# Optimization experiments

Hardware: AMD Instinct MI355X
Metric: run time of the kernel (lower is better)

## Reference

```python
import jax, jax.numpy as jnp
import numpy as np

B, T, I, H, BB, O = 128, 1024, 64, 512, 128, 2  # batch, time, input, hidden, backbone_units, phys outputs

def _lecun_tanh(v):
    return 1.7159 * jnp.tanh(0.666 * v)

def setup_inputs() -> dict:
    key = jax.random.key(0)
    ks = jax.random.split(key, 20)
    s = lambda fan_in: 1.0 / np.sqrt(fan_in)
    def lin(k, out_d, in_d):
        return jax.random.uniform(k, (out_d, in_d), jnp.float32, -s(in_d), s(in_d))
    def bias(k, out_d, in_d):
        return jax.random.uniform(k, (out_d,), jnp.float32, -s(in_d), s(in_d))
    return {
        "x": jax.random.normal(ks[0], (B, T, I), jnp.float32),
        # ncps LSTMCell: input_map Linear(I,4H,bias=True), recurrent_map Linear(H,4H,bias=False)
        "lstm_Wi": lin(ks[1], 4 * H, I),
        "lstm_bi": bias(ks[2], 4 * H, I),
        "lstm_Wh": lin(ks[3], 4 * H, H),
        # CfCCell backbone: Linear(I+H, BB) + lecun_tanh
        "bb_W": lin(ks[4], BB, I + H),
        "bb_b": bias(ks[5], BB, I + H),
        # ff1/ff2/time_a/time_b: Linear(BB, H)
        "ff1_W": lin(ks[6], H, BB), "ff1_b": bias(ks[7], H, BB),
        "ff2_W": lin(ks[8], H, BB), "ff2_b": bias(ks[9], H, BB),
        "ta_W": lin(ks[10], H, BB), "ta_b": bias(ks[11], H, BB),
        "tb_W": lin(ks[12], H, BB), "tb_b": bias(ks[13], H, BB),
        # PhysicsHead: Linear(H, O)
        "head_W": lin(ks[14], O, H), "head_b": bias(ks[15], O, H),
    }

def _cfc_scan(x, lstm_Wi, lstm_bi, lstm_Wh, bb_W, bb_b,
              ff1_W, ff1_b, ff2_W, ff2_b, ta_W, ta_b, tb_W, tb_b):
    Bsz = x.shape[0]
    Hd = ff1_W.shape[0]
    ts = jnp.float32(1.0)  # default elapsed time per step in ncps CfC

    def step(carry, xt):
        h, c = carry
        # mixed-memory LSTM gate (forget-gate bias +1.0, per ncps)
        z = xt @ lstm_Wi.T + lstm_bi + h @ lstm_Wh.T
        i_, ig, fg, og = jnp.split(z, 4, axis=-1)
        c_new = c * jax.nn.sigmoid(fg + 1.0) + jnp.tanh(i_) * jax.nn.sigmoid(ig)
        h_lstm = jnp.tanh(c_new) * jax.nn.sigmoid(og)
        # CfC cell (mode='default') on [input, lstm_hidden]
        f = _lecun_tanh(jnp.concatenate([xt, h_lstm], axis=-1) @ bb_W.T + bb_b)
        ff1 = jnp.tanh(f @ ff1_W.T + ff1_b)
        ff2 = jnp.tanh(f @ ff2_W.T + ff2_b)
        t_interp = jax.nn.sigmoid((f @ ta_W.T + ta_b) * ts + (f @ tb_W.T + tb_b))
        h_new = ff1 * (1.0 - t_interp) + t_interp * ff2
        return (h_new, c_new), h_new

    h0 = jnp.zeros((Bsz, Hd), x.dtype)
    c0 = jnp.zeros((Bsz, Hd), x.dtype)
    (h_last, _), h_seq = jax.lax.scan(step, (h0, c0), jnp.swapaxes(x, 0, 1))
    return jnp.swapaxes(h_seq, 0, 1), h_last  # (B,T,H), (B,H)

def reference(x, lstm_Wi, lstm_bi, lstm_Wh, bb_W, bb_b,
              ff1_W, ff1_b, ff2_W, ff2_b, ta_W, ta_b, tb_W, tb_b,
              head_W, head_b):
    h_seq, last_h = _cfc_scan(x, lstm_Wi, lstm_bi, lstm_Wh, bb_W, bb_b,
                              ff1_W, ff1_b, ff2_W, ff2_b, ta_W, ta_b, tb_W, tb_b)
    phys_pred = h_seq @ head_W.T + head_b  # (B,T,O)
    return phys_pred, last_h
```

## Files before the change

kernel.cpp:

```cpp
#include <hip/hip_runtime.h>

#define NB 128
#define TT 1024
#define DI 64
#define DH 512
#define DB 128
#define GZ 2048
#define KZ 576
#define BST 136

typedef unsigned short u16;
typedef unsigned char u8;
typedef unsigned int u32;
typedef unsigned long long u64;

#if defined(__has_builtin)
#if __has_builtin(__builtin_amdgcn_fdot2)
#define HAS_FDOT2 1
#endif
#if __has_builtin(__builtin_amdgcn_sdot4)
#define HAS_SDOT4 1
#endif
#endif

typedef _Float16 half2v __attribute__((ext_vector_type(2)));

__device__ __forceinline__ float bf2f(u16 u) {
  union { u32 i; float f; } v; v.i = ((u32)u) << 16; return v.f;
}
__device__ __forceinline__ float fsig(float x) {
  return __builtin_amdgcn_rcpf(1.f + __expf(-x));
}
__device__ __forceinline__ float ftanh(float x) {
  return 1.f - 2.f * __builtin_amdgcn_rcpf(__expf(2.f * x) + 1.f);
}
__device__ __forceinline__ float dot2p(u32 w, u32 a, float acc) {
#ifdef HAS_FDOT2
  return __builtin_amdgcn_fdot2(__builtin_bit_cast(half2v, w),
                                __builtin_bit_cast(half2v, a), acc, false);
#else
  half2v hw = __builtin_bit_cast(half2v, w), ha = __builtin_bit_cast(half2v, a);
  acc = fmaf((float)hw.x, (float)ha.x, acc);
  return fmaf((float)hw.y, (float)ha.y, acc);
#endif
}
__device__ __forceinline__ int dot4i(u32 w, u32 a, int acc) {
#ifdef HAS_SDOT4
  return __builtin_amdgcn_sdot4((int)w, (int)a, acc, false);
#else
  acc += (((int)(w << 24)) >> 24) * (((int)(a << 24)) >> 24);
  acc += (((int)(w << 16)) >> 24) * (((int)(a << 16)) >> 24);
  acc += (((int)(w << 8))  >> 24) * (((int)(a << 8))  >> 24);
  acc += (((int)w) >> 24)         * (((int)a) >> 24);
  return acc;
#endif
}
__device__ __forceinline__ u32 packf16(float x, float y) {
  half2v h; h.x = (_Float16)x; h.y = (_Float16)y;
  return __builtin_bit_cast(u32, h);
}
__device__ __forceinline__ u16 f16b(float x) {
  _Float16 h = (_Float16)x;
  return __builtin_bit_cast(u16, h);
}

#define O_WZX  256
#define O_WZ8  (O_WZX + 262144)
#define O_SWZ  (O_WZ8 + 1048576)
#define O_BB8  (O_SWZ + 8192)
#define O_SBB  (O_BB8 + 73728)
#define O_FF8  (O_SBB + 512)
#define O_SFF  (O_FF8 + 262144)
#define O_BIF  (O_SFF + 8192)
#define O_FFB  (O_BIF + 8192)
#define O_BBBF (O_FFB + 8192)
#define O_HWP  (O_BBBF + 512)
#define O_HBF  (O_HWP + 2048)
#define WS_NEED ((u64)(O_HBF + 256))

__global__ void detect_kernel(const u16* x, const u16* wi, const u16* wh, int* flag) {
  const int l = threadIdx.x;
  int cnt = (((x[2 * l] >> 7) & 0xFF) < 134)
          + (((wi[2 * l] >> 7) & 0xFF) < 134)
          + (((wh[2 * l] >> 7) & 0xFF) < 134);
#pragma unroll
  for (int off = 32; off > 0; off >>= 1) cnt += __shfl_down(cnt, off, 64);
  if (l == 0) *flag = (cnt >= 180) ? 1 : 0;
}

__device__ __forceinline__ float ldf(int f, const void* s, u32 i) {
  return f ? bf2f(((const u16*)s)[i]) : ((const float*)s)[i];
}

__global__ void pwzx_kernel(const void* Wi, const int* __restrict__ flag,
                            u32* __restrict__ wzxG) {
  const int o = blockIdx.x * 256 + threadIdx.x;
  const int k2 = blockIdx.y;
  const int f = *flag;
  const u32 i = (u32)o * DI + 2 * k2;
  wzxG[(u32)k2 * GZ + (((u32)(o & 511)) << 2) + (o >> 9)] =
      packf16(ldf(f, Wi, i), ldf(f, Wi, i + 1));
}

__global__ void qwz_kernel(const void* Wh, const int* __restrict__ flag,
                           u32* __restrict__ wzG, float* __restrict__ swzG) {
  const int o = blockIdx.x;
  const int l = threadIdx.x;
  const int f = *flag;
  float w[8]; float mx = 0.f;
#pragma unroll
  for (int qq = 0; qq < 2; ++qq) {
    const int q = l + 64 * qq;
#pragma unroll
    for (int e = 0; e < 4; ++e) {
      const float v = ldf(f, Wh, (u32)o * DH + 4 * q + e);
      w[qq * 4 + e] = v; mx = fmaxf(mx, fabsf(v));
    }
  }
#pragma unroll
  for (int off = 32; off > 0; off >>= 1) mx = fmaxf(mx, __shfl_xor(mx, off, 64));
  mx = fmaxf(mx, 1e-20f);
  const float inv = 127.f / mx;
  if (l == 0) swzG[(((u32)(o & 511)) << 2) + (o >> 9)] = mx / (127.f * 127.f);
#pragma unroll
  for (int qq = 0; qq < 2; ++qq) {
    const int q = l + 64 * qq;
    u32 p = 0;
#pragma unroll
    for (int e = 0; e < 4; ++e) {
      int b = (int)rintf(w[qq * 4 + e] * inv);
      b = b > 127 ? 127 : (b < -127 ? -127 : b);
      p |= ((u32)(b & 0xff)) << (8 * e);
    }
    wzG[(u32)q * GZ + (((u32)(o & 511)) << 2) + (o >> 9)] = p;
  }
}

__global__ void qbb_kernel(const void* bb, const int* __restrict__ flag,
                           u32* __restrict__ bb8, float* __restrict__ sbb) {
  const int m = blockIdx.x;
  const int l = threadIdx.x;
  const int f = *flag;
  float mx = 0.f;
#pragma unroll
  for (int q = 0; q < 9; ++q)
    mx = fmaxf(mx, fabsf(ldf(f, bb, (u32)m * KZ + l + 64 * q)));
#pragma unroll
  for (int off = 32; off > 0; off >>= 1) mx = fmaxf(mx, __shfl_xor(mx, off, 64));
  mx = fmaxf(mx, 1e-20f);
  const float inv = 127.f / mx;
  if (l == 0) sbb[m] = mx / 127.f;
  for (int k4 = l; k4 < 144; k4 += 64) {
    u32 p = 0;
#pragma unroll
    for (int e = 0; e < 4; ++e) {
      int b = (int)rintf(ldf(f, bb, (u32)m * KZ + 4 * k4 + e) * inv);
      b = b > 127 ? 127 : (b < -127 ? -127 : b);
      p |= ((u32)(b & 0xff)) << (8 * e);
    }
    bb8[(u32)k4 * DB + m] = p;
  }
}

__global__ void qff_kernel(const void* f1, const void* f2, const void* ta,
                           const void* tb, const int* __restrict__ flag,
                           u32* __restrict__ ffG, float* __restrict__ sffG) {
  const int o = blockIdx.x;
  const int mat = blockIdx.y;
  const int l = threadIdx.x;
  const void* s = (mat == 0) ? f1 : (mat == 1) ? f2 : (mat == 2) ? ta : tb;
  const int f = *flag;
  float w[4]; float mx = 0.f;
#pragma unroll
  for (int e = 0; e < 4; ++e) {
    w[e] = ldf(f, s, (u32)o * DB + 4 * l + e);
    mx = fmaxf(mx, fabsf(w[e]));
  }
#pragma unroll
  for (int off = 16; off > 0; off >>= 1) mx = fmaxf(mx, __shfl_xor(mx, off, 32));
  mx = fmaxf(mx, 1e-20f);
  const float inv = 127.f / mx;
  if (l == 0) sffG[((u32)o << 2) + mat] = (mx / 127.f) * (1.7159f / 127.f);
  u32 p = 0;
#pragma unroll
  for (int e = 0; e < 4; ++e) {
    int b = (int)rintf(w[e] * inv);
    b = b > 127 ? 127 : (b < -127 ? -127 : b);
    p |= ((u32)(b & 0xff)) << (8 * e);
  }
  ffG[(((u32)l * 512 + o) << 2) + mat] = p;
}

__global__ void psmall_kernel(const void* bi_s, const void* f1b_s, const void* f2b_s,
                              const void* tab_s, const void* tbb_s, const void* bbb_s,
                              const void* hw_s, const void* hb_s,
                              const int* __restrict__ flag,
                              float* __restrict__ bif, float* __restrict__ ffb,
                              float* __restrict__ bbbf, u32* __restrict__ hwp,
                              float* __restrict__ hbf) {
  const int f = *flag;
  for (int i = threadIdx.x; i < 2048; i += 1024) {
    bif[i] = ldf(f, bi_s, i);
    if (i < 512) {
      ffb[i]        = ldf(f, f1b_s, i);
      ffb[512 + i]  = ldf(f, f2b_s, i);
      ffb[1024 + i] = ldf(f, tab_s, i);
      ffb[1536 + i] = ldf(f, tbb_s, i);
      const int w = i >> 8, pr = i & 255;
      hwp[i] = packf16(ldf(f, hw_s, w * DH + 2 * pr), ldf(f, hw_s, w * DH + 2 * pr + 1));
    }
    if (i < 128) bbbf[i] = ldf(f, bbb_s, i);
    if (i < 2)   hbf[i] = ldf(f, hb_s, i);
  }
}

__global__ __launch_bounds__(1024, 1)
void scan18(const void* __restrict__ xraw, const int* __restrict__ flagp,
            const u32* __restrict__ wzxG, const u32* __restrict__ wzG,
            const float* __restrict__ swzG,
            const u32* __restrict__ bb8, const float* __restrict__ sbb,
            const u32* __restrict__ ffG, const float* __restrict__ sffG,
            const float* __restrict__ bif, const float* __restrict__ ffbv,
            const float* __restrict__ bbbf, const u32* __restrict__ hwp,
            const float* __restrict__ hbf, float* __restrict__ out)
{
  __shared__ __align__(16) u32   xf16q[32];
  __shared__ __align__(16) u32   ah8q[128];
  __shared__ __align__(16) u32   hfR[256];
  __shared__ __align__(16) u32   vcat8[144];
  __shared__ __align__(16) float sxq[4];
  __shared__ __align__(16) u32   Fq8[32];
  __shared__ __align__(16) u32   bbL[144 * BST + 1024];

  const int j = threadIdx.x;
  const int b = blockIdx.x;
  const int bf16in = *flagp;
  const int u = j & 511;

  float c0 = 0.f;
  float bgi = 0, bgg = 0, bgf = 0, bgo = 0, cb1 = 0, cb2 = 0, cba = 0, cbb = 0;
  float4 zscl = make_float4(0, 0, 0, 0), sfv = make_float4(0, 0, 0, 0);
  if (j < 512) {
    bgi = bif[0 * DH + u]; bgg = bif[1 * DH + u];
    bgf = bif[2 * DH + u]; bgo = bif[3 * DH + u];
    cb1 = ffbv[0 * DH + u]; cb2 = ffbv[1 * DH + u];
    cba = ffbv[2 * DH + u]; cbb = ffbv[3 * DH + u];
    zscl = *(const float4*)(swzG + 4 * u);
    sfv  = *(const float4*)(sffG + 4 * u);
  }
  float sbbr = 0.f, bbr = 0.f;
  if (j < 512) { sbbr = sbb[j >> 2]; bbr = bbbf[j >> 2]; }
  u32 hwreg[4] = {0, 0, 0, 0}; float hbr = 0.f;
  int hw_ = 0, hl = 0;
  if (j >= 576 && j < 704) {
    const int jj = j - 576;
    hw_ = jj >> 6; hl = jj & 63;
#pragma unroll
    for (int i = 0; i < 4; ++i) hwreg[i] = hwp[hw_ * 256 + hl + 64 * i];
    hbr = hbf[hw_];
  }
  const float C127 = 1.f / 127.f;

  for (int idx = j; idx < 144 * DB; idx += 1024) {
    const int q = idx >> 7, m = idx & 127;
    bbL[q * BST + m] = bb8[idx];
  }

  if (j < 256) { hfR[j] = 0u; if (j < 128) ah8q[j] = 0u; }
  if (j >= 512 && j < 544) {
    const int k2 = j - 512;
    const size_t xi = ((size_t)b * TT + 0) * 32 + k2;
    float a, bb_;
    if (bf16in) {
      const u32 w = ((const u32*)xraw)[xi];
      a = bf2f((u16)(w & 0xffffu)); bb_ = bf2f((u16)(w >> 16));
    } else {
      const float2 v = ((const float2*)xraw)[xi];
      a = v.x; bb_ = v.y;
    }
    xf16q[k2] = packf16(a, bb_);
    float m = fmaxf(fabsf(a), fabsf(bb_));
#pragma unroll
    for (int off = 16; off > 0; off >>= 1) m = fmaxf(m, __shfl_xor(m, off, 32));
    m = fmaxf(m, 1e-20f);
    if (k2 == 0) sxq[0] = m * C127;
    const float inv = 127.f / m;
    const int q0 = (int)rintf(a * inv), q1 = (int)rintf(bb_ * inv);
    ((u16*)vcat8)[k2] = (u16)((q0 & 0xff) | ((q1 & 0xff) << 8));
  }
  __syncthreads();

  for (int t = 0; t < TT; ++t) {
    if (j < 512) {
      float xi0 = 0, xg0 = 0, xf0 = 0, xo0 = 0;
      const u32* wpx = wzxG + 4 * u;
#pragma unroll 8
      for (int k2 = 0; k2 < 32; ++k2) {
        const uint4 w = *(const uint4*)wpx; wpx += GZ;
        const u32 a0 = xf16q[k2];
        xi0 = dot2p(w.x, a0, xi0); xg0 = dot2p(w.y, a0, xg0);
        xf0 = dot2p(w.z, a0, xf0); xo0 = dot2p(w.w, a0, xo0);
      }
      int ii0 = 0, ig0 = 0, if0 = 0, io0 = 0;
      const u32* wph = wzG + 4 * u;
#pragma unroll 8
      for (int q = 0; q < 128; ++q) {
        const uint4 w = *(const uint4*)wph; wph += GZ;
        const u32 a0 = ah8q[q];
        ii0 = dot4i(w.x, a0, ii0); ig0 = dot4i(w.y, a0, ig0);
        if0 = dot4i(w.z, a0, if0); io0 = dot4i(w.w, a0, io0);
      }
      const float zi0 = bgi + xi0 + zscl.x * (float)ii0;
      const float zg0 = bgg + xg0 + zscl.y * (float)ig0;
      const float zf0 = bgf + xf0 + zscl.z * (float)if0;
      const float zo0 = bgo + xo0 + zscl.w * (float)io0;
      c0 = fmaf(c0, fsig(zf0 + 1.f), ftanh(zi0) * fsig(zg0));
      const float hl0 = ftanh(c0) * fsig(zo0);
      const int q0 = (int)rintf(hl0 * 127.f);
      ((u8*)vcat8)[64 + u] = (u8)(q0 & 0xff);
    }
    __syncthreads();

    if (j < 512) {
      const int m = j >> 2, s4 = j & 3;
      const int qb = s4 * 36;
      int ax0 = 0, ah0 = 0;
#pragma unroll 12
      for (int q = 0; q < 36; ++q) {
        const int qq = qb + q;
        const u32 w = bbL[qq * BST + m];
        const int d0 = dot4i(w, vcat8[qq], 0);
        const bool isx = qq < 16;
        ax0 += isx ? d0 : 0; ah0 += isx ? 0 : d0;
      }
      ax0 += __shfl_xor(ax0, 1, 64); ax0 += __shfl_xor(ax0, 2, 64);
      ah0 += __shfl_xor(ah0, 1, 64); ah0 += __shfl_xor(ah0, 2, 64);
      if (s4 == 0) {
        const float r0 = bbr + sbbr * (sxq[0] * (float)ax0 + C127 * (float)ah0);
        const float F0 = 1.7159f * ftanh(0.666f * r0);
        const int q0 = (int)rintf(F0 * (127.f / 1.7159f));
        ((u8*)Fq8)[m] = (u8)(q0 & 0xff);
      }
    }
    __syncthreads();

    if (j < 512) {
      int a10 = 0, a20 = 0, aa0 = 0, ab0 = 0;
      const u32* fw = ffG + 4 * u;
#pragma unroll 8
      for (int l = 0; l < 32; ++l) {
        const uint4 w = *(const uint4*)fw; fw += GZ;
        const u32 F0v = Fq8[l];
        a10 = dot4i(w.x, F0v, a10); a20 = dot4i(w.y, F0v, a20);
        aa0 = dot4i(w.z, F0v, aa0); ab0 = dot4i(w.w, F0v, ab0);
      }
      const float z10 = sfv.x * (float)a10 + cb1, z20 = sfv.y * (float)a20 + cb2;
      const float za0 = sfv.z * (float)aa0 + cba, zb0 = sfv.w * (float)ab0 + cbb;
      const float ti0 = fsig(za0 + zb0);
      const float hn0 = fmaf(ftanh(z10), 1.f - ti0, ti0 * ftanh(z20));
      ((u16*)hfR)[u] = f16b(hn0);
      const int q0 = (int)rintf(hn0 * 127.f);
      ((u8*)ah8q)[u] = (u8)(q0 & 0xff);
      if (t == TT - 1) {
        out[(size_t)NB * TT * 2 + (size_t)b * DH + u] = hn0;
      }
    } else if (j < 544 && t + 1 < TT) {
      const int k2 = j - 512;
      const size_t xi = ((size_t)b * TT + (t + 1)) * 32 + k2;
      float a, bb_;
      if (bf16in) {
        const u32 w = ((const u32*)xraw)[xi];
        a = bf2f((u16)(w & 0xffffu)); bb_ = bf2f((u16)(w >> 16));
      } else {
        const float2 v = ((const float2*)xraw)[xi];
        a = v.x; bb_ = v.y;
      }
      xf16q[k2] = packf16(a, bb_);
      float m = fmaxf(fabsf(a), fabsf(bb_));
#pragma unroll
      for (int off = 16; off > 0; off >>= 1) m = fmaxf(m, __shfl_xor(m, off, 32));
      m = fmaxf(m, 1e-20f);
      if (k2 == 0) sxq[0] = m * C127;
      const float inv = 127.f / m;
      const int q0 = (int)rintf(a * inv), q1 = (int)rintf(bb_ * inv);
      ((u16*)vcat8)[k2] = (u16)((q0 & 0xff) | ((q1 & 0xff) << 8));
    }
    __syncthreads();

    if (j >= 576 && j < 704) {
      float acc = 0.f;
#pragma unroll
      for (int i = 0; i < 4; ++i)
        acc = dot2p(hwreg[i], hfR[hl + 64 * i], acc);
#pragma unroll
      for (int off = 32; off > 0; off >>= 1) acc += __shfl_down(acc, off, 64);
      if (hl == 0) out[((size_t)b * TT + t) * 2 + hw_] = acc + hbr;
    }
  }
}

__device__ __forceinline__ void fma8(float& acc, const uint4 u, const float* v) {
  union { u32 i; float f; } tt;
  tt.i = u.x << 16;          acc = fmaf(tt.f, v[0], acc);
  tt.i = u.x & 0xffff0000u;  acc = fmaf(tt.f, v[1], acc);
  tt.i = u.y << 16;          acc = fmaf(tt.f, v[2], acc);
  tt.i = u.y & 0xffff0000u;  acc = fmaf(tt.f, v[3], acc);
  tt.i = u.z << 16;          acc = fmaf(tt.f, v[4], acc);
  tt.i = u.z & 0xffff0000u;  acc = fmaf(tt.f, v[5], acc);
  tt.i = u.w << 16;          acc = fmaf(tt.f, v[6], acc);
  tt.i = u.w & 0xffff0000u;  acc = fmaf(tt.f, v[7], acc);
}
__global__ __launch_bounds__(256, 1)
void fb_scan(const u16* __restrict__ x,   const u16* __restrict__ Wi,
             const u16* __restrict__ bi,  const u16* __restrict__ Wh,
             const u16* __restrict__ bbW, const u16* __restrict__ bbb,
             const u16* __restrict__ f1W, const u16* __restrict__ f1b,
             const u16* __restrict__ f2W, const u16* __restrict__ f2b,
             const u16* __restrict__ taW, const u16* __restrict__ tab,
             const u16* __restrict__ tbW, const u16* __restrict__ tbb,
             const u16* __restrict__ hW,  const u16* __restrict__ hb,
             float* __restrict__ out)
{
  __shared__ __align__(16) float vcat[DI + DH];
  __shared__ __align__(16) float Fb2[DB];
  __shared__ __align__(16) float fpart[256];
  __shared__ __align__(16) float hprev[DH];
  const int j = threadIdx.x, b = blockIdx.x;
  const int u0 = j, u1 = j + 256;
  float bi_r[8];
#pragma unroll
  for (int k = 0; k < 8; ++k) bi_r[k] = bf2f(bi[j + 256 * k]);
  const float b_f1_0 = bf2f(f1b[u0]), b_f1_1 = bf2f(f1b[u1]);
  const float b_f2_0 = bf2f(f2b[u0]), b_f2_1 = bf2f(f2b[u1]);
  const float b_ta_0 = bf2f(tab[u0]), b_ta_1 = bf2f(tab[u1]);
  const float b_tb_0 = bf2f(tbb[u0]), b_tb_1 = bf2f(tbb[u1]);
  const float b_bb = (j < DB) ? bf2f(bbb[j]) : 0.f;
  float hwr[8]; float hbr = 0.f;
  if (j < 128) {
    const int w = j >> 6, l = j & 63;
#pragma unroll
    for (int q = 0; q < 8; ++q) hwr[q] = bf2f(hW[w * DH + q * 64 + l]);
    hbr = bf2f(hb[w]);
  }
  float c0 = 0.f, c1 = 0.f;
  hprev[u0] = 0.f; hprev[u1] = 0.f;
  const u16* xp = x + (size_t)b * TT * DI;
  __syncthreads();
  for (int t = 0; t < TT; ++t) {
    if (j < DI) vcat[j] = bf2f(xp[t * DI + j]);
    __syncthreads();
    float a[8];
#pragma unroll
    for (int k = 0; k < 8; ++k) a[k] = bi_r[k];
#pragma unroll
    for (int r = 0; r < 8; ++r) {
      const u16* wr = Wi + ((size_t)(j + 256 * r)) * DI;
      float acc = a[r];
#pragma unroll
      for (int kk = 0; kk < DI; kk += 8) fma8(acc, *(const uint4*)(wr + kk), vcat + kk);
      a[r] = acc;
    }
#pragma unroll 1
    for (int kb = 0; kb < DH; kb += 64) {
      float hreg[64];
#pragma unroll
      for (int q = 0; q < 16; ++q)
        *(float4*)(hreg + 4 * q) = *(const float4*)(hprev + kb + 4 * q);
#pragma unroll
      for (int r = 0; r < 8; ++r) {
        const u16* wr = Wh + ((size_t)(j + 256 * r)) * DH + kb;
        float acc = a[r];
#pragma unroll
        for (int cc = 0; cc < 8; ++cc) fma8(acc, *(const uint4*)(wr + 8 * cc), hreg + 8 * cc);
        a[r] = acc;
      }
    }
    {
      const float cn0 = fmaf(c0, fsig(a[4] + 1.f), ftanh(a[0]) * fsig(a[2]));
      const float cn1 = fmaf(c1, fsig(a[5] + 1.f), ftanh(a[1]) * fsig(a[3]));
      c0 = cn0; c1 = cn1;
      vcat[DI + u0] = ftanh(cn0) * fsig(a[6]);
      vcat[DI + u1] = ftanh(cn1) * fsig(a[7]);
    }
    __syncthreads();
    {
      const int mm = j & (DB - 1), pp = j >> 7;
      const u16* br = bbW + (size_t)mm * KZ + pp * 288;
      const float* vs = vcat + pp * 288;
      float s0 = 0.f, s1 = 0.f, s2v = 0.f, s3 = 0.f;
#pragma unroll
      for (int kk = 0; kk < 288; kk += 32) {
        fma8(s0, *(const uint4*)(br + kk), vs + kk);
        fma8(s1, *(const uint4*)(br + kk + 8), vs + kk + 8);
        fma8(s2v, *(const uint4*)(br + kk + 16), vs + kk + 16);
        fma8(s3, *(const uint4*)(br + kk + 24), vs + kk + 24);
      }
      fpart[j] = (s0 + s1) + (s2v + s3);
    }
    __syncthreads();
    if (j < DB) Fb2[j] = 1.7159f * ftanh(0.666f * (b_bb + fpart[j] + fpart[j + DB]));
    __syncthreads();
    {
      float Fr[DB];
#pragma unroll
      for (int q = 0; q < 32; ++q) *(float4*)(Fr + 4 * q) = *(const float4*)(Fb2 + 4 * q);
      const u16* rp[8] = {
        f1W + (size_t)u0 * DB, f1W + (size_t)u1 * DB,
        f2W + (size_t)u0 * DB, f2W + (size_t)u1 * DB,
        taW + (size_t)u0 * DB, taW + (size_t)u1 * DB,
        tbW + (size_t)u0 * DB, tbW + (size_t)u1 * DB };
      float sacc[8] = { b_f1_0, b_f1_1, b_f2_0, b_f2_1, b_ta_0, b_ta_1, b_tb_0, b_tb_1 };
#pragma unroll
      for (int rr = 0; rr < 8; ++rr) {
        float acc = sacc[rr];
        const u16* r = rp[rr];
#pragma unroll
        for (int kk = 0; kk < DB; kk += 8) fma8(acc, *(const uint4*)(r + kk), Fr + kk);
        sacc[rr] = acc;
      }
      const float ti0 = fsig(sacc[4] + sacc[6]);
      const float ti1 = fsig(sacc[5] + sacc[7]);
      hprev[u0] = fmaf(ftanh(sacc[0]), 1.f - ti0, ti0 * ftanh(sacc[2]));
      hprev[u1] = fmaf(ftanh(sacc[1]), 1.f - ti1, ti1 * ftanh(sacc[3]));
    }
    __syncthreads();
    if (j < 128) {
      const int l = j & 63;
      float acc = 0.f;
#pragma unroll
      for (int q = 0; q < 8; ++q) acc = fmaf(hprev[q * 64 + l], hwr[q], acc);
#pragma unroll
      for (int off = 32; off > 0; off >>= 1) acc += __shfl_down(acc, off, 64);
      if (l == 0) out[((size_t)b * TT + t) * 2 + (j >> 6)] = acc + hbr;
    }
  }
  out[(size_t)NB * TT * 2 + (size_t)b * DH + u0] = hprev[u0];
  out[(size_t)NB * TT * 2 + (size_t)b * DH + u1] = hprev[u1];
}

extern "C" void kernel_launch(void* const* d_in, const int* in_sizes, int n_in,
                              void* d_out, int out_size, void* d_ws, size_t ws_size,
                              hipStream_t stream) {
  (void)in_sizes; (void)n_in; (void)out_size;

  if (ws_size >= WS_NEED) {
    char* ws = (char*)d_ws;
    int* flag = (int*)ws;
    detect_kernel<<<dim3(1), dim3(64), 0, stream>>>(
        (const u16*)d_in[0], (const u16*)d_in[1], (const u16*)d_in[3], flag);
    pwzx_kernel<<<dim3(8, 32), dim3(256), 0, stream>>>(d_in[1], flag, (u32*)(ws + O_WZX));
    qwz_kernel<<<dim3(2048), dim3(64), 0, stream>>>(d_in[3], flag,
                                                    (u32*)(ws + O_WZ8), (float*)(ws + O_SWZ));
    qbb_kernel<<<dim3(128), dim3(64), 0, stream>>>(d_in[4], flag,
                                                   (u32*)(ws + O_BB8), (float*)(ws + O_SBB));
    qff_kernel<<<dim3(512, 4), dim3(32), 0, stream>>>(d_in[6], d_in[8], d_in[10],
                                                      d_in[12], flag,
                                                      (u32*)(ws + O_FF8), (float*)(ws + O_SFF));
    psmall_kernel<<<dim3(1), dim3(1024), 0, stream>>>(
        d_in[2], d_in[7], d_in[9], d_in[11], d_in[13], d_in[5], d_in[14], d_in[15],
        flag, (float*)(ws + O_BIF), (float*)(ws + O_FFB), (float*)(ws + O_BBBF),
        (u32*)(ws + O_HWP), (float*)(ws + O_HBF));

    scan18<<<dim3(128), dim3(1024), 0, stream>>>(
        d_in[0], flag,
        (const u32*)(ws + O_WZX), (const u32*)(ws + O_WZ8), (const float*)(ws + O_SWZ),
        (const u32*)(ws + O_BB8), (const float*)(ws + O_SBB),
        (const u32*)(ws + O_FF8), (const float*)(ws + O_SFF),
        (const float*)(ws + O_BIF), (const float*)(ws + O_FFB),
        (const float*)(ws + O_BBBF), (const u32*)(ws + O_HWP),
        (const float*)(ws + O_HBF), (float*)d_out);
  } else {
    fb_scan<<<dim3(NB), dim3(256), 0, stream>>>(
        (const u16*)d_in[0],  (const u16*)d_in[1],  (const u16*)d_in[2],
        (const u16*)d_in[3],  (const u16*)d_in[4],  (const u16*)d_in[5],
        (const u16*)d_in[6],  (const u16*)d_in[7],  (const u16*)d_in[8],
        (const u16*)d_in[9],  (const u16*)d_in[10], (const u16*)d_in[11],
        (const u16*)d_in[12], (const u16*)d_in[13], (const u16*)d_in[14],
        (const u16*)d_in[15], (float*)d_out);
  }
}
```

Measured before the change: 13.20 ms.

## Compute input projection for two timesteps per weight load and separate x/h backbone buffers

The x@Wi projection now runs every other step and computes both the current and next timestep from the same global weight loads, keeping the next step's result in registers. This halves weight streaming for that part of the recurrence. The x prefetch moves two steps ahead into a 4-slot ring buffer so both steps' inputs are ready. The backbone dot product now uses separate x-int8 and h-int8 buffers with split loops, which removes the per-iteration select. The cost is more registers per thread and an uneven amount of work on odd and even steps.

```diff
diff --git a/kernel.cpp b/kernel.cpp
--- a/kernel.cpp
+++ b/kernel.cpp
@@ -215,7 +215,7 @@
 }
 
 __global__ __launch_bounds__(1024, 1)
-void scan18(const void* __restrict__ xraw, const int* __restrict__ flagp,
+void scan19(const void* __restrict__ xraw, const int* __restrict__ flagp,
             const u32* __restrict__ wzxG, const u32* __restrict__ wzG,
             const float* __restrict__ swzG,
             const u32* __restrict__ bb8, const float* __restrict__ sbb,
@@ -224,10 +224,11 @@
             const float* __restrict__ bbbf, const u32* __restrict__ hwp,
             const float* __restrict__ hbf, float* __restrict__ out)
 {
-  __shared__ __align__(16) u32   xf16q[32];
+  __shared__ __align__(16) u32   xf16q[128];
+  __shared__ __align__(16) u32   xi8q[64];
+  __shared__ __align__(16) u32   hl8q[128];
   __shared__ __align__(16) u32   ah8q[128];
   __shared__ __align__(16) u32   hfR[256];
-  __shared__ __align__(16) u32   vcat8[144];
   __shared__ __align__(16) float sxq[4];
   __shared__ __align__(16) u32   Fq8[32];
   __shared__ __align__(16) u32   bbL[144 * BST + 1024];
@@ -238,6 +239,7 @@
   const int u = j & 511;
 
   float c0 = 0.f;
+  float sxi = 0.f, sxg = 0.f, sxf = 0.f, sxo = 0.f;
   float bgi = 0, bgg = 0, bgf = 0, bgo = 0, cb1 = 0, cb2 = 0, cba = 0, cbb = 0;
   float4 zscl = make_float4(0, 0, 0, 0), sfv = make_float4(0, 0, 0, 0);
   if (j < 512) {
@@ -267,9 +269,9 @@
   }
 
   if (j < 256) { hfR[j] = 0u; if (j < 128) ah8q[j] = 0u; }
-  if (j >= 512 && j < 544) {
-    const int k2 = j - 512;
-    const size_t xi = ((size_t)b * TT + 0) * 32 + k2;
+  if (j >= 512 && j < 576) {
+    const int s = (j - 512) >> 5, k2 = (j - 512) & 31;
+    const size_t xi = ((size_t)b * TT + s) * 32 + k2;
     float a, bb_;
     if (bf16in) {
       const u32 w = ((const u32*)xraw)[xi];
@@ -278,29 +280,20 @@
       const float2 v = ((const float2*)xraw)[xi];
       a = v.x; bb_ = v.y;
     }
-    xf16q[k2] = packf16(a, bb_);
+    xf16q[s * 32 + k2] = packf16(a, bb_);
     float m = fmaxf(fabsf(a), fabsf(bb_));
 #pragma unroll
     for (int off = 16; off > 0; off >>= 1) m = fmaxf(m, __shfl_xor(m, off, 32));
     m = fmaxf(m, 1e-20f);
-    if (k2 == 0) sxq[0] = m * C127;
+    if (k2 == 0) sxq[s] = m * C127;
     const float inv = 127.f / m;
     const int q0 = (int)rintf(a * inv), q1 = (int)rintf(bb_ * inv);
-    ((u16*)vcat8)[k2] = (u16)((q0 & 0xff) | ((q1 & 0xff) << 8));
+    ((u16*)xi8q)[s * 32 + k2] = (u16)((q0 & 0xff) | ((q1 & 0xff) << 8));
   }
   __syncthreads();
 
   for (int t = 0; t < TT; ++t) {
     if (j < 512) {
-      float xi0 = 0, xg0 = 0, xf0 = 0, xo0 = 0;
-      const u32* wpx = wzxG + 4 * u;
-#pragma unroll 8
-      for (int k2 = 0; k2 < 32; ++k2) {
-        const uint4 w = *(const uint4*)wpx; wpx += GZ;
-        const u32 a0 = xf16q[k2];
-        xi0 = dot2p(w.x, a0, xi0); xg0 = dot2p(w.y, a0, xg0);
-        xf0 = dot2p(w.z, a0, xf0); xo0 = dot2p(w.w, a0, xo0);
-      }
       int ii0 = 0, ig0 = 0, if0 = 0, io0 = 0;
       const u32* wph = wzG + 4 * u;
 #pragma unroll 8
@@ -310,6 +303,26 @@
         ii0 = dot4i(w.x, a0, ii0); ig0 = dot4i(w.y, a0, ig0);
         if0 = dot4i(w.z, a0, if0); io0 = dot4i(w.w, a0, io0);
       }
+      float xi0, xg0, xf0, xo0;
+      if ((t & 1) == 0) {
+        xi0 = 0; xg0 = 0; xf0 = 0; xo0 = 0;
+        float xiN = 0, xgN = 0, xfN = 0, xoN = 0;
+        const u32* wpx = wzxG + 4 * u;
+        const u32* xc = xf16q + (t & 3) * 32;
+        const u32* xn = xf16q + ((t + 1) & 3) * 32;
+#pragma unroll 8
+        for (int k2 = 0; k2 < 32; ++k2) {
+          const uint4 w = *(const uint4*)wpx; wpx += GZ;
+          const u32 a0 = xc[k2], a1 = xn[k2];
+          xi0 = dot2p(w.x, a0, xi0); xg0 = dot2p(w.y, a0, xg0);
+          xf0 = dot2p(w.z, a0, xf0); xo0 = dot2p(w.w, a0, xo0);
+          xiN = dot2p(w.x, a1, xiN); xgN = dot2p(w.y, a1, xgN);
+          xfN = dot2p(w.z, a1, xfN); xoN = dot2p(w.w, a1, xoN);
+        }
+        sxi = xiN; sxg = xgN; sxf = xfN; sxo = xoN;
+      } else {
+        xi0 = sxi; xg0 = sxg; xf0 = sxf; xo0 = sxo;
+      }
       const float zi0 = bgi + xi0 + zscl.x * (float)ii0;
       const float zg0 = bgg + xg0 + zscl.y * (float)ig0;
       const float zf0 = bgf + xf0 + zscl.z * (float)if0;
@@ -317,26 +330,28 @@
       c0 = fmaf(c0, fsig(zf0 + 1.f), ftanh(zi0) * fsig(zg0));
       const float hl0 = ftanh(c0) * fsig(zo0);
       const int q0 = (int)rintf(hl0 * 127.f);
-      ((u8*)vcat8)[64 + u] = (u8)(q0 & 0xff);
+      ((u8*)hl8q)[u] = (u8)(q0 & 0xff);
     }
     __syncthreads();
 
     if (j < 512) {
       const int m = j >> 2, s4 = j & 3;
-      const int qb = s4 * 36;
       int ax0 = 0, ah0 = 0;
-#pragma unroll 12
-      for (int q = 0; q < 36; ++q) {
-        const int qq = qb + q;
-        const u32 w = bbL[qq * BST + m];
-        const int d0 = dot4i(w, vcat8[qq], 0);
-        const bool isx = qq < 16;
-        ax0 += isx ? d0 : 0; ah0 += isx ? 0 : d0;
+      const u32* xq = xi8q + (t & 3) * 16;
+#pragma unroll
+      for (int q = 0; q < 4; ++q) {
+        const int qq = 4 * q + s4;
+        ax0 = dot4i(bbL[qq * BST + m], xq[qq], ax0);
+      }
+#pragma unroll 8
+      for (int q = 4; q < 36; ++q) {
+        const int qq = 4 * q + s4;
+        ah0 = dot4i(bbL[qq * BST + m], hl8q[qq - 16], ah0);
       }
       ax0 += __shfl_xor(ax0, 1, 64); ax0 += __shfl_xor(ax0, 2, 64);
       ah0 += __shfl_xor(ah0, 1, 64); ah0 += __shfl_xor(ah0, 2, 64);
       if (s4 == 0) {
-        const float r0 = bbr + sbbr * (sxq[0] * (float)ax0 + C127 * (float)ah0);
+        const float r0 = bbr + sbbr * (sxq[t & 3] * (float)ax0 + C127 * (float)ah0);
         const float F0 = 1.7159f * ftanh(0.666f * r0);
         const int q0 = (int)rintf(F0 * (127.f / 1.7159f));
         ((u8*)Fq8)[m] = (u8)(q0 & 0xff);
@@ -364,9 +379,10 @@
       if (t == TT - 1) {
         out[(size_t)NB * TT * 2 + (size_t)b * DH + u] = hn0;
       }
-    } else if (j < 544 && t + 1 < TT) {
+    } else if (j < 544 && t + 2 < TT) {
       const int k2 = j - 512;
-      const size_t xi = ((size_t)b * TT + (t + 1)) * 32 + k2;
+      const int slot = (t + 2) & 3;
+      const size_t xi = ((size_t)b * TT + (t + 2)) * 32 + k2;
       float a, bb_;
       if (bf16in) {
         const u32 w = ((const u32*)xraw)[xi];
@@ -375,15 +391,15 @@
         const float2 v = ((const float2*)xraw)[xi];
         a = v.x; bb_ = v.y;
       }
-      xf16q[k2] = packf16(a, bb_);
+      xf16q[slot * 32 + k2] = packf16(a, bb_);
       float m = fmaxf(fabsf(a), fabsf(bb_));
 #pragma unroll
       for (int off = 16; off > 0; off >>= 1) m = fmaxf(m, __shfl_xor(m, off, 32));
       m = fmaxf(m, 1e-20f);
-      if (k2 == 0) sxq[0] = m * C127;
+      if (k2 == 0) sxq[slot] = m * C127;
       const float inv = 127.f / m;
       const int q0 = (int)rintf(a * inv), q1 = (int)rintf(bb_ * inv);
-      ((u16*)vcat8)[k2] = (u16)((q0 & 0xff) | ((q1 & 0xff) << 8));
+      ((u16*)xi8q)[slot * 32 + k2] = (u16)((q0 & 0xff) | ((q1 & 0xff) << 8));
     }
     __syncthreads();
 
@@ -561,7 +577,7 @@
         flag, (float*)(ws + O_BIF), (float*)(ws + O_FFB), (float*)(ws + O_BBBF),
         (u32*)(ws + O_HWP), (float*)(ws + O_HBF));
 
-    scan18<<<dim3(128), dim3(1024), 0, stream>>>(
+    scan19<<<dim3(128), dim3(1024), 0, stream>>>(
         d_in[0], flag,
         (const u32*)(ws + O_WZX), (const u32*)(ws + O_WZ8), (const float*)(ws + O_SWZ),
         (const u32*)(ws + O_BB8), (const float*)(ws + O_SBB),
```

New measurement: 11.82 ms. -10.5%, faster.
